# Optimization experiments

Hardware: AMD Instinct MI355X
Metric: run time of the kernel (lower is better)

Reference implementation:

```python
import jax, jax.numpy as jnp
import numpy as np

KS = 3  # kernel size (mask semantics hardcode 3x3 = 9 taps)


def _xy2d(n, x, y):
    # Hilbert curve: 2D coords -> 1D distance (exact port of HilbertTopology.xy2d)
    d = 0
    s = n // 2
    while s > 0:
        rx = 1 if (x & s) > 0 else 0
        ry = 1 if (y & s) > 0 else 0
        d += s * s * ((3 * rx) ^ ry)
        # rot(s, x, y, rx, ry)
        if ry == 0:
            if rx == 1:
                x = s - 1 - x
                y = s - 1 - y
            x, y = y, x
        s //= 2
    return d


def _build_causal_mask(height, width):
    n = 1
    while n < max(width, height):
        n *= 2
    hgrid = np.empty((height, width), dtype=np.int64)
    for y in range(height):
        for x in range(width):
            hgrid[y, x] = _xy2d(n, x, y)
    # pad with -1 so out-of-bounds neighbors never mask (mask stays 1.0, matching torch code)
    hp = np.pad(hgrid, 1, constant_values=-1)
    mask = np.ones((KS * KS, height, width), dtype=np.float32)
    k = 0
    for dy in range(KS):
        for dx in range(KS):
            nh = hp[dy:dy + height, dx:dx + width]
            mask[k] = np.where(nh > hgrid, 0.0, 1.0)
            k += 1
    return mask[None, None]  # [1, 1, 9, H, W]


def setup_inputs() -> dict:
    key = jax.random.key(0)
    k1, k2 = jax.random.split(key)
    B, C, H, W = 4, 256, 128, 128
    retina = jax.random.normal(k1, (B, C, H, W), dtype=jnp.float32)
    evolve_weight = jax.random.normal(k2, (C, C, KS, KS), dtype=jnp.float32) * 0.05
    causal_mask = jnp.asarray(_build_causal_mask(H, W))
    return {"retina": retina, "evolve_weight": evolve_weight,
            "causal_mask": causal_mask, "steps": 5}


def _spatial_causal_conv(x, evolve_weight, causal_mask):
    B, C, H, W = x.shape
    xp = jnp.pad(x, ((0, 0), (0, 0), (1, 1), (1, 1)))
    # im2col in F.unfold's (dy, dx) tap order -> [B, C, 9, H, W]
    patches = jnp.stack([xp[:, :, dy:dy + H, dx:dx + W]
                         for dy in range(KS) for dx in range(KS)], axis=2)
    masked = patches * causal_mask  # position-dependent causal mask
    w = evolve_weight.reshape(C, C * KS * KS)
    out = jnp.einsum('oj,bjhw->bohw', w, masked.reshape(B, C * KS * KS, H, W))
    return out


def reference(retina, evolve_weight, causal_mask, steps):
    x = retina
    for _ in range(steps):
        delta = _spatial_causal_conv(x, evolve_weight, causal_mask)
        x = x + delta / (1.0 + jnp.abs(delta))  # exact_activation
    return x
```

## Files before the change

### kernel.cpp

```cpp
#include <hip/hip_runtime.h>
#include <math.h>
#include <stdint.h>

#define B_ 4
#define C_ 256
#define H_ 128
#define W_ 128
#define NPIX (H_*W_)

typedef short bf16x8 __attribute__((ext_vector_type(8)));
typedef int   i32x4  __attribute__((ext_vector_type(4)));
typedef float f32x4  __attribute__((ext_vector_type(4)));
typedef float f32x16 __attribute__((ext_vector_type(16)));
typedef unsigned short u16x4 __attribute__((ext_vector_type(4)));

#define XSZ   41984
#define WOFF  (2*XSZ)
#define WSL   32768
#define SCR   (WOFF + 2*WSL)
#define LDS_TOTAL (SCR + 1024)

__device__ __forceinline__ unsigned short f2bf_rne(float v) {
    uint32_t b = __float_as_uint(v);
    return (unsigned short)((b + 0x7fff + ((b >> 16) & 1)) >> 16);
}
__device__ __forceinline__ float bf2f(unsigned short h) {
    return __uint_as_float(((uint32_t)h) << 16);
}

__global__ __launch_bounds__(256)
void prep_w(const float* __restrict__ wg, unsigned short* __restrict__ wb,
            unsigned short* __restrict__ zb) {
    if (blockIdx.x == 2304) { if (threadIdx.x < 128) zb[threadIdx.x] = 0; return; }
    int f = blockIdx.x * 256 + threadIdx.x;
    int sl = f >> 14, within = f & 16383;
    int o = within >> 6, t = within & 63;
    int up = t >> 3, e = t & 7;
    int qt = sl / 9, k = sl - qt * 9;
    int c = qt * 64 + ((up ^ (o & 7)) << 3) + e;
    wb[f] = f2bf_rne(wg[(o * C_ + c) * 9 + k]);
}

__global__ __launch_bounds__(256)
void prep_split(const float* __restrict__ retina, unsigned short* __restrict__ hi,
                unsigned short* __restrict__ lo) {
    __shared__ unsigned int t[64][65];
    int bid = blockIdx.x;
    const int wt = bid & 1;        bid >>= 1;
    const int h  = bid & 127;      bid >>= 7;
    const int ct = bid & 3;        const int b = bid >> 2;
    const int tid = threadIdx.x;
    const int ci4 = tid >> 6, wi = tid & 63;
    #pragma unroll
    for (int cc = 0; cc < 16; ++cc) {
        int c_loc = cc * 4 + ci4;
        float v = retina[((size_t)(b * C_ + ct * 64 + c_loc) * H_ + h) * W_ + wt * 64 + wi];
        unsigned short hv = f2bf_rne(v);
        unsigned short lv = f2bf_rne(v - bf2f(hv));
        t[c_loc][wi] = (unsigned)hv | ((unsigned)lv << 16);
    }
    __syncthreads();
    const int p = tid >> 2, j = tid & 3;
    size_t base = (((size_t)(b * H_ + h) * W_ + wt * 64 + p) << 8) + ct * 64 + j * 16;
    u16x4 hv4[4], lv4[4];
    #pragma unroll
    for (int e = 0; e < 16; ++e) {
        unsigned u = t[j * 16 + e][p];
        hv4[e >> 2][e & 3] = (unsigned short)(u & 0xffffu);
        lv4[e >> 2][e & 3] = (unsigned short)(u >> 16);
    }
    #pragma unroll
    for (int q2 = 0; q2 < 4; ++q2) {
        *(u16x4*)(hi + base + q2 * 4) = hv4[q2];
        *(u16x4*)(lo + base + q2 * 4) = lv4[q2];
    }
}

__device__ __forceinline__ void stage_w(const unsigned short* __restrict__ wb_all,
                                        char* smem, int woff, int sl, int wid, int l) {
    const char* src = (const char*)wb_all + ((size_t)sl << 15);
    #pragma unroll
    for (int j = 0; j < 4; ++j) {
        const int seg = ((j << 3) + wid) << 10;
        __builtin_amdgcn_global_load_lds(
            (const __attribute__((address_space(1))) uint32_t*)(src + seg + l * 16),
            (__attribute__((address_space(3))) uint32_t*)(smem + woff + seg), 16, 0, 0);
    }
    __builtin_amdgcn_sched_barrier(0);
}

__device__ __forceinline__ void stage_x(const unsigned short* __restrict__ hi_in,
                                        const unsigned short* __restrict__ zb,
                                        char* smem, int xoff, int b, int tr, int tc,
                                        int qt, int wid, int l) {
    const int slot_r = l >> 3, sub = l & 7;
    #pragma unroll
    for (int op = 0; op < 6; ++op) {
        const int sbase = (op << 6) + (wid << 3);
        const int s = sbase + slot_r;
        const int rr = (s * 3641) >> 16;
        const int hc = s - rr * 18;
        const int h = tr * 16 + rr - 1;
        const int w = tc * 16 + hc - 1;
        const unsigned short* src;
        int dst;
        if (sbase < 328) {
            dst = xoff + (sbase << 7);
            if ((unsigned)h < 128u && (unsigned)w < 128u)
                src = hi_in + ((((size_t)(b * 128 + h) << 7) + w) << 8) + (qt << 6)
                            + ((sub ^ (s & 7)) << 3);
            else
                src = zb + (sub << 3);
        } else {
            dst = SCR;
            src = zb + (sub << 3);
        }
        __builtin_amdgcn_global_load_lds(
            (const __attribute__((address_space(1))) uint32_t*)src,
            (__attribute__((address_space(3))) uint32_t*)(smem + dst), 16, 0, 0);
    }
    __builtin_amdgcn_sched_barrier(0);
}

__global__ __launch_bounds__(512, 2)
void nca_v7(const unsigned short* __restrict__ hi_in,
            const unsigned short* __restrict__ lo_in,
            const unsigned short* __restrict__ wb,
            const unsigned short* __restrict__ zb,
            const float* __restrict__ mask,
            unsigned short* __restrict__ hi_out,
            unsigned short* __restrict__ lo_out)
{
    extern __shared__ char smem[];
    const int tid = threadIdx.x;
    const int l = tid & 63, wid = tid >> 6;
    const int wave_o = wid & 1, wave_p = wid >> 1;
    const int lane31 = l & 31, khalf = l >> 5;
    const int col = l & 15, rowin = (l >> 4) & 1;

    int bid = blockIdx.x;
    const int tc = bid & 7; bid >>= 3;
    const int tr = bid & 7; const int b = bid >> 3;

    unsigned mbits = 0;
    #pragma unroll
    for (int k = 0; k < 9; ++k) {
        #pragma unroll
        for (int n = 0; n < 2; ++n) {
            const int h = tr * 16 + wave_p * 4 + n * 2 + rowin;
            const int w = tc * 16 + col;
            unsigned bit = (mask[k * NPIX + h * W_ + w] != 0.f) ? 1u : 0u;
            mbits |= bit << (k * 2 + n);
        }
    }
    __builtin_amdgcn_sched_barrier(0);

    stage_w(wb, smem, WOFF,       0, wid, l);
    stage_w(wb, smem, WOFF + WSL, 1, wid, l);
    stage_x(hi_in, zb, smem, 0,   b, tr, tc, 0, wid, l);
    stage_x(hi_in, zb, smem, XSZ, b, tr, tc, 1, wid, l);

    int sB[2];
    #pragma unroll
    for (int n = 0; n < 2; ++n) sB[n] = (wave_p * 4 + n * 2 + rowin) * 18 + col;
    int abase[4], aswz[4];
    #pragma unroll
    for (int mo = 0; mo < 4; ++mo) {
        int o_l = wave_o * 128 + mo * 32 + lane31;
        abase[mo] = o_l << 7;
        aswz[mo] = o_l & 7;
    }

    f32x16 zv;
    #pragma unroll
    for (int r = 0; r < 16; ++r) zv[r] = 0.f;
    f32x16 acc[4][2];
    #pragma unroll
    for (int mo = 0; mo < 4; ++mo)
        #pragma unroll
        for (int n = 0; n < 2; ++n) acc[mo][n] = zv;

    #pragma unroll 1
    for (int qt = 0; qt < 4; ++qt) {
        const char* xbuf = smem + ((qt & 1) ? XSZ : 0);
        #pragma unroll 1
        for (int k = 0; k < 9; ++k) {
            const int sl = qt * 9 + k;
            if (qt == 0 && k <= 1)                   asm volatile("s_waitcnt vmcnt(6)"  ::: "memory");
            else if ((qt == 1 || qt == 2) && k <= 1) asm volatile("s_waitcnt vmcnt(10)" ::: "memory");
            else if (sl == 35)                       asm volatile("s_waitcnt vmcnt(0)"  ::: "memory");
            else                                     asm volatile("s_waitcnt vmcnt(4)"  ::: "memory");
            __builtin_amdgcn_sched_barrier(0);
            __builtin_amdgcn_s_barrier();

            const int dy = (k * 11) >> 5;
            const int dx = k - dy * 3;
            const int doff = dy * 18 + dx;
            const char* wbuf = smem + WOFF + ((sl & 1) ? WSL : 0);
            const unsigned mk = mbits >> (k * 2);

            int sx[2];
            #pragma unroll
            for (int n = 0; n < 2; ++n) sx[n] = sB[n] + doff;

            __builtin_amdgcn_s_setprio(1);
            #pragma unroll
            for (int ks = 0; ks < 4; ++ks) {
                const int ua = ks * 2 + khalf;
                bf16x8 av[4];
                #pragma unroll
                for (int mo = 0; mo < 4; ++mo)
                    av[mo] = *(const bf16x8*)(wbuf + abase[mo] + ((ua ^ aswz[mo]) << 4));
                bf16x8 bv[2];
                #pragma unroll
                for (int n = 0; n < 2; ++n) {
                    i32x4 braw = *(const i32x4*)(xbuf + sx[n] * 128 + ((ua ^ (sx[n] & 7)) << 4));
                    const int mm = -(int)((mk >> n) & 1u);
                    #pragma unroll
                    for (int w4 = 0; w4 < 4; ++w4) braw[w4] &= mm;
                    bv[n] = __builtin_bit_cast(bf16x8, braw);
                }
                #pragma unroll
                for (int mo = 0; mo < 4; ++mo)
                    #pragma unroll
                    for (int n = 0; n < 2; ++n)
                        acc[mo][n] = __builtin_amdgcn_mfma_f32_32x32x16_bf16(av[mo], bv[n], acc[mo][n], 0, 0, 0);
            }
            __builtin_amdgcn_s_setprio(0);

            asm volatile("" ::: "memory");
            __builtin_amdgcn_s_barrier();
            if (sl + 2 < 36)
                stage_w(wb, smem, WOFF + ((sl & 1) ? WSL : 0), sl + 2, wid, l);
            if (k == 8 && qt < 2)
                stage_x(hi_in, zb, smem, (qt & 1) ? XSZ : 0, b, tr, tc, qt + 2, wid, l);
        }
    }

    __syncthreads();
    #pragma unroll
    for (int ph = 0; ph < 2; ++ph) {
        if ((wave_p >> 1) == ph) {
            #pragma unroll
            for (int mo = 0; mo < 4; ++mo) {
                #pragma unroll
                for (int n = 0; n < 2; ++n) {
                    const int row_local = (wave_p & 1) * 4 + n * 2 + rowin;
                    const int pl = row_local * 16 + col;
                    #pragma unroll
                    for (int rq = 0; rq < 4; ++rq) {
                        const int u = wave_o * 32 + mo * 8 + rq * 2 + khalf;
                        f32x4 v;
                        v[0] = acc[mo][n][rq * 4 + 0];
                        v[1] = acc[mo][n][rq * 4 + 1];
                        v[2] = acc[mo][n][rq * 4 + 2];
                        v[3] = acc[mo][n][rq * 4 + 3];
                        *(f32x4*)(smem + pl * 1024 + ((u ^ (pl & 7)) << 4)) = v;
                    }
                }
            }
        }
        __syncthreads();
        #pragma unroll 2
        for (int it = 0; it < 16; ++it) {
            const int pl = it * 8 + wid;
            const int h = tr * 16 + ph * 8 + (pl >> 4);
            const int w = tc * 16 + (pl & 15);
            const f32x4 d4 = *(const f32x4*)(smem + pl * 1024 + ((l ^ wid) << 4));
            const size_t base = (((size_t)((b * 128 + h) * 128 + w)) << 8) + l * 4;
            const u16x4 h4 = *(const u16x4*)(hi_in + base);
            const u16x4 l4 = *(const u16x4*)(lo_in + base);
            u16x4 ho, lo2;
            #pragma unroll
            for (int r = 0; r < 4; ++r) {
                const float xv = bf2f(h4[r]) + bf2f(l4[r]);
                const float d = d4[r];
                const float xn = xv + d / (1.f + fabsf(d));
                ho[r] = f2bf_rne(xn);
                lo2[r] = f2bf_rne(xn - bf2f(ho[r]));
            }
            *(u16x4*)(hi_out + base) = ho;
            *(u16x4*)(lo_out + base) = lo2;
        }
        if (ph == 0) __syncthreads();
    }
}

__global__ __launch_bounds__(256)
void shadows_to_f32(const unsigned short* __restrict__ hi,
                    const unsigned short* __restrict__ lo,
                    float* __restrict__ out)
{
    __shared__ float t[64][132];
    int bid = blockIdx.x;
    const int ct = bid & 3;  bid >>= 2;
    const int h  = bid & 127; const int b = bid >> 7;
    const int tid = threadIdx.x;
    #pragma unroll
    for (int pass = 0; pass < 8; ++pass) {
        const int w = pass * 16 + (tid >> 4);
        const int c0 = (tid & 15) * 4;
        const size_t base = (((size_t)((b * 128 + h) * 128 + w)) << 8) + ct * 64 + c0;
        const u16x4 hv = *(const u16x4*)(hi + base);
        const u16x4 lv = *(const u16x4*)(lo + base);
        #pragma unroll
        for (int e = 0; e < 4; ++e) t[c0 + e][w] = bf2f(hv[e]) + bf2f(lv[e]);
    }
    __syncthreads();
    #pragma unroll
    for (int pass = 0; pass < 8; ++pass) {
        const int c = pass * 8 + (tid >> 5);
        const int w = (tid & 31) * 4;
        float4 v = make_float4(t[c][w], t[c][w + 1], t[c][w + 2], t[c][w + 3]);
        *(float4*)(out + ((size_t)(b * C_ + ct * 64 + c) * H_ + h) * W_ + w) = v;
    }
}

#define OT 64
#define TR 4
#define TC 16
#define CKC 16
__global__ __launch_bounds__(256)
void nca_step_f32(const float* __restrict__ xin, const float* __restrict__ wg,
                  const float* __restrict__ mask, float* __restrict__ xout)
{
    __shared__ __align__(16) float w_s[CKC][9][OT];
    __shared__ __align__(16) float x_s[CKC][TR + 2][20];
    const int tid = threadIdx.x;
    int bt = blockIdx.x;
    const int col_tile = bt & 7;  bt >>= 3;
    const int row_tile = bt & 31; bt >>= 5;
    const int ot = bt & 3;        const int b = bt >> 2;
    const int gr0 = row_tile * TR, gc0 = col_tile * TC, o_base = ot * OT;
    const int og = tid >> 4, pg = tid & 15;
    const int prow = pg >> 2, pcol4 = (pg & 3) * 4;
    const int orow = gr0 + prow, ocol0 = gc0 + pcol4;
    float mask_r[9][4];
// ... 43 lines not shown
#pragma unroll
                    for (int j = 0; j < 4; ++j) acck[dxx][a][j] = 0.f;
#pragma unroll 4
            for (int c = 0; c < CKC; ++c) {
                const float4 xv4 = *(const float4*)&x_s[c][prow + dyy][pcol4];
                const float2 xv2 = *(const float2*)&x_s[c][prow + dyy][pcol4 + 4];
                const float xv[6] = {xv4.x, xv4.y, xv4.z, xv4.w, xv2.x, xv2.y};
#pragma unroll
                for (int dxx = 0; dxx < 3; ++dxx) {
                    const float4 wv = *(const float4*)&w_s[c][dyy * 3 + dxx][og * 4];
                    const float wa[4] = {wv.x, wv.y, wv.z, wv.w};
#pragma unroll
                    for (int a = 0; a < 4; ++a)
#pragma unroll
                        for (int j = 0; j < 4; ++j)
                            acck[dxx][a][j] = fmaf(wa[a], xv[j + dxx], acck[dxx][a][j]);
                }
            }
#pragma unroll
            for (int dxx = 0; dxx < 3; ++dxx) {
                const int k = dyy * 3 + dxx;
#pragma unroll
                for (int a = 0; a < 4; ++a)
#pragma unroll
                    for (int j = 0; j < 4; ++j)
                        acc[a][j] = fmaf(mask_r[k][j], acck[dxx][a][j], acc[a][j]);
            }
        }
        __syncthreads();
    }
#pragma unroll
    for (int a = 0; a < 4; ++a) {
        const int o = o_base + og * 4 + a;
#pragma unroll
        for (int j = 0; j < 4; ++j) {
            const int idx = ((b * C_ + o) * H_ + orow) * W_ + (ocol0 + j);
            const float d = acc[a][j];
            xout[idx] = xin[idx] + d / (1.0f + fabsf(d));
        }
    }
}

extern "C" void kernel_launch(void* const* d_in, const int* in_sizes, int n_in,
                              void* d_out, int out_size, void* d_ws, size_t ws_size,
                              hipStream_t stream) {
    const float* retina = (const float*)d_in[0];
    const float* wg     = (const float*)d_in[1];
    const float* mask   = (const float*)d_in[2];
    float* out = (float*)d_out;

    const size_t need = 0x4200000;

    if (ws_size >= need) {
        unsigned short* wb  = (unsigned short*)d_ws;
        unsigned short* zb  = (unsigned short*)((char*)d_ws + 0x120000);
        unsigned short* hiA = (unsigned short*)((char*)d_ws + 0x200000);
        unsigned short* loA = (unsigned short*)((char*)d_ws + 0x2200000);
        unsigned short* hiB = (unsigned short*)d_out;
        unsigned short* loB = hiB + (size_t)B_ * NPIX * C_;

        hipFuncSetAttribute((const void*)nca_v7,
                            hipFuncAttributeMaxDynamicSharedMemorySize, LDS_TOTAL);

        prep_w<<<2305, 256, 0, stream>>>(wg, wb, zb);
        prep_split<<<4096, 256, 0, stream>>>(retina, hiB, loB);

        nca_v7<<<256, 512, LDS_TOTAL, stream>>>(hiB, loB, wb, zb, mask, hiA, loA);
        nca_v7<<<256, 512, LDS_TOTAL, stream>>>(hiA, loA, wb, zb, mask, hiB, loB);
        nca_v7<<<256, 512, LDS_TOTAL, stream>>>(hiB, loB, wb, zb, mask, hiA, loA);
        nca_v7<<<256, 512, LDS_TOTAL, stream>>>(hiA, loA, wb, zb, mask, hiB, loB);
        nca_v7<<<256, 512, LDS_TOTAL, stream>>>(hiB, loB, wb, zb, mask, hiA, loA);
        shadows_to_f32<<<2048, 256, 0, stream>>>(hiA, loA, out);
    } else {
        float* ws = (float*)d_ws;
        const int nblocks = B_ * (C_ / OT) * (H_ / TR) * (W_ / TC);
        const float* src = retina;
        float* dsts[5] = {out, ws, out, ws, out};
        for (int s = 0; s < 5; ++s) {
            nca_step_f32<<<dim3(nblocks), dim3(256), 0, stream>>>(src, wg, mask, dsts[s]);
            src = dsts[s];
        }
    }
}
```

Measured before the change: 484.4 us.

## Load weight fragments directly into registers instead of staging through LDS

Weights are repacked into an MFMA-fragment-ready layout so each wave loads its A operands straight from global memory into registers, double-buffered two slices ahead. This removes LDS weight staging and most per-slice barriers. Waves are re-partitioned to 64 output channels by 64 pixels (2x4 MFMA tiles), and the epilogue writes in four quarter passes. The cost is higher register pressure and heavier global/L2 weight traffic per wave, plus fully unrolled code.

```diff
diff --git a/kernel.cpp b/kernel.cpp
--- a/kernel.cpp
+++ b/kernel.cpp
@@ -15,9 +15,7 @@
 typedef unsigned short u16x4 __attribute__((ext_vector_type(4)));
 
 #define XSZ   41984
-#define WOFF  (2*XSZ)
-#define WSL   32768
-#define SCR   (WOFF + 2*WSL)
+#define SCR   (2*XSZ)
 #define LDS_TOTAL (SCR + 1024)
 
 __device__ __forceinline__ unsigned short f2bf_rne(float v) {
@@ -29,16 +27,23 @@
 }
 
 __global__ __launch_bounds__(256)
-void prep_w(const float* __restrict__ wg, unsigned short* __restrict__ wb,
-            unsigned short* __restrict__ zb) {
+void prep_w2(const float* __restrict__ wg, unsigned short* __restrict__ wb2,
+             unsigned short* __restrict__ zb) {
     if (blockIdx.x == 2304) { if (threadIdx.x < 128) zb[threadIdx.x] = 0; return; }
     int f = blockIdx.x * 256 + threadIdx.x;
-    int sl = f >> 14, within = f & 16383;
-    int o = within >> 6, t = within & 63;
-    int up = t >> 3, e = t & 7;
+    int sl = f >> 14;
+    int r = f & 16383;
+    int oq = r >> 12;  r &= 4095;
+    int mo = r >> 11;  r &= 2047;
+    int ks = r >> 9;   r &= 511;
+    int kh = r >> 8;
+    int o5 = (r >> 3) & 31;
+    int e  = r & 7;
+    int o = oq * 64 + mo * 32 + o5;
+    int u = ks * 2 + kh;
     int qt = sl / 9, k = sl - qt * 9;
-    int c = qt * 64 + ((up ^ (o & 7)) << 3) + e;
-    wb[f] = f2bf_rne(wg[(o * C_ + c) * 9 + k]);
+    int c = qt * 64 + u * 8 + e;
+    wb2[f] = f2bf_rne(wg[(o * C_ + c) * 9 + k]);
 }
 
 __global__ __launch_bounds__(256)
@@ -74,19 +79,6 @@
         *(u16x4*)(hi + base + q2 * 4) = hv4[q2];
         *(u16x4*)(lo + base + q2 * 4) = lv4[q2];
     }
-}
-
-__device__ __forceinline__ void stage_w(const unsigned short* __restrict__ wb_all,
-                                        char* smem, int woff, int sl, int wid, int l) {
-    const char* src = (const char*)wb_all + ((size_t)sl << 15);
-    #pragma unroll
-    for (int j = 0; j < 4; ++j) {
-        const int seg = ((j << 3) + wid) << 10;
-        __builtin_amdgcn_global_load_lds(
-            (const __attribute__((address_space(1))) uint32_t*)(src + seg + l * 16),
-            (__attribute__((address_space(3))) uint32_t*)(smem + woff + seg), 16, 0, 0);
-    }
-    __builtin_amdgcn_sched_barrier(0);
 }
 
 __device__ __forceinline__ void stage_x(const unsigned short* __restrict__ hi_in,
@@ -122,10 +114,12 @@
     __builtin_amdgcn_sched_barrier(0);
 }
 
+struct Aset { bf16x8 f[2][4]; };
+
 __global__ __launch_bounds__(512, 2)
-void nca_v7(const unsigned short* __restrict__ hi_in,
+void nca_v8(const unsigned short* __restrict__ hi_in,
             const unsigned short* __restrict__ lo_in,
-            const unsigned short* __restrict__ wb,
+            const unsigned short* __restrict__ wb2,
             const unsigned short* __restrict__ zb,
             const float* __restrict__ mask,
             unsigned short* __restrict__ hi_out,
@@ -134,155 +128,154 @@
     extern __shared__ char smem[];
     const int tid = threadIdx.x;
     const int l = tid & 63, wid = tid >> 6;
-    const int wave_o = wid & 1, wave_p = wid >> 1;
-    const int lane31 = l & 31, khalf = l >> 5;
+    const int oq = wid & 3, ph2 = wid >> 2;
+    const int khalf = l >> 5;
     const int col = l & 15, rowin = (l >> 4) & 1;
 
     int bid = blockIdx.x;
     const int tc = bid & 7; bid >>= 3;
     const int tr = bid & 7; const int b = bid >> 3;
 
-    unsigned mbits = 0;
+    unsigned long long mbits = 0ull;
     #pragma unroll
     for (int k = 0; k < 9; ++k) {
         #pragma unroll
-        for (int n = 0; n < 2; ++n) {
-            const int h = tr * 16 + wave_p * 4 + n * 2 + rowin;
+        for (int n = 0; n < 4; ++n) {
+            const int h = tr * 16 + ph2 * 8 + n * 2 + rowin;
             const int w = tc * 16 + col;
-            unsigned bit = (mask[k * NPIX + h * W_ + w] != 0.f) ? 1u : 0u;
-            mbits |= bit << (k * 2 + n);
+            unsigned long long bit = (mask[k * NPIX + h * W_ + w] != 0.f) ? 1ull : 0ull;
+            mbits |= bit << (k * 4 + n);
         }
     }
     __builtin_amdgcn_sched_barrier(0);
 
-    stage_w(wb, smem, WOFF,       0, wid, l);
-    stage_w(wb, smem, WOFF + WSL, 1, wid, l);
     stage_x(hi_in, zb, smem, 0,   b, tr, tc, 0, wid, l);
     stage_x(hi_in, zb, smem, XSZ, b, tr, tc, 1, wid, l);
 
-    int sB[2];
-    #pragma unroll
-    for (int n = 0; n < 2; ++n) sB[n] = (wave_p * 4 + n * 2 + rowin) * 18 + col;
-    int abase[4], aswz[4];
-    #pragma unroll
-    for (int mo = 0; mo < 4; ++mo) {
-        int o_l = wave_o * 128 + mo * 32 + lane31;
-        abase[mo] = o_l << 7;
-        aswz[mo] = o_l & 7;
-    }
+    const char* abase = (const char*)wb2 + (oq << 13) + (l << 4);
+    Aset a0, a1;
+    #pragma unroll
+    for (int mo = 0; mo < 2; ++mo)
+        #pragma unroll
+        for (int ks = 0; ks < 4; ++ks) {
+            a0.f[mo][ks] = *(const bf16x8*)(abase +     0 + mo * 4096 + ks * 1024);
+            a1.f[mo][ks] = *(const bf16x8*)(abase + 32768 + mo * 4096 + ks * 1024);
+        }
+    asm volatile("s_waitcnt vmcnt(16)" ::: "memory");
+    __builtin_amdgcn_sched_barrier(0);
+    __builtin_amdgcn_s_barrier();
+
+    int sB[4];
+    #pragma unroll
+    for (int n = 0; n < 4; ++n) sB[n] = (ph2 * 8 + n * 2 + rowin) * 18 + col;
 
     f32x16 zv;
     #pragma unroll
     for (int r = 0; r < 16; ++r) zv[r] = 0.f;
-    f32x16 acc[4][2];
-    #pragma unroll
-    for (int mo = 0; mo < 4; ++mo)
+    f32x16 acc[2][4];
+    #pragma unroll
+    for (int mo = 0; mo < 2; ++mo)
         #pragma unroll
-        for (int n = 0; n < 2; ++n) acc[mo][n] = zv;
-
-    #pragma unroll 1
-    for (int qt = 0; qt < 4; ++qt) {
+        for (int n = 0; n < 4; ++n) acc[mo][n] = zv;
+
+    #pragma unroll
+    for (int sl = 0; sl < 36; ++sl) {
+        const int qt = sl / 9, k = sl - qt * 9;
+        const int dy = k / 3, dx = k - dy * 3;
+        const int doff = dy * 18 + dx;
         const char* xbuf = smem + ((qt & 1) ? XSZ : 0);
-        #pragma unroll 1
-        for (int k = 0; k < 9; ++k) {
-            const int sl = qt * 9 + k;
-            if (qt == 0 && k <= 1)                   asm volatile("s_waitcnt vmcnt(6)"  ::: "memory");
-            else if ((qt == 1 || qt == 2) && k <= 1) asm volatile("s_waitcnt vmcnt(10)" ::: "memory");
-            else if (sl == 35)                       asm volatile("s_waitcnt vmcnt(0)"  ::: "memory");
-            else                                     asm volatile("s_waitcnt vmcnt(4)"  ::: "memory");
+        const unsigned mk = (unsigned)(mbits >> (k * 4));
+        Aset& cur = (sl & 1) ? a1 : a0;
+
+        __builtin_amdgcn_s_setprio(1);
+        #pragma unroll
+        for (int ks = 0; ks < 4; ++ks) {
+            const int u = ks * 2 + khalf;
+            bf16x8 bv[4];
+            #pragma unroll
+            for (int n = 0; n < 4; ++n) {
+                const int spx = sB[n] + doff;
+                i32x4 braw = *(const i32x4*)(xbuf + spx * 128 + ((u ^ (spx & 7)) << 4));
+                const int mm = -(int)((mk >> n) & 1u);
+                #pragma unroll
+                for (int w4 = 0; w4 < 4; ++w4) braw[w4] &= mm;
+                bv[n] = __builtin_bit_cast(bf16x8, braw);
+            }
+            #pragma unroll
+            for (int mo = 0; mo < 2; ++mo)
+                #pragma unroll
+                for (int n = 0; n < 4; ++n)
+                    acc[mo][n] = __builtin_amdgcn_mfma_f32_32x32x16_bf16(cur.f[mo][ks], bv[n], acc[mo][n], 0, 0, 0);
+        }
+        __builtin_amdgcn_s_setprio(0);
+
+        if (sl + 2 < 36) {
+            const char* base2 = abase + (size_t)(sl + 2) * 32768;
+            #pragma unroll
+            for (int mo = 0; mo < 2; ++mo)
+                #pragma unroll
+                for (int ks = 0; ks < 4; ++ks)
+                    cur.f[mo][ks] = *(const bf16x8*)(base2 + mo * 4096 + ks * 1024);
+        }
+        if (k == 4 && (qt == 1 || qt == 2))
+            stage_x(hi_in, zb, smem, ((qt + 1) & 1) ? XSZ : 0, b, tr, tc, qt + 1, wid, l);
+        if (k == 8 && qt < 3) {
+            __builtin_amdgcn_sched_barrier(0);
+            if (qt >= 1) { asm volatile("s_waitcnt vmcnt(24)" ::: "memory"); }
             __builtin_amdgcn_sched_barrier(0);
             __builtin_amdgcn_s_barrier();
-
-            const int dy = (k * 11) >> 5;
-            const int dx = k - dy * 3;
-            const int doff = dy * 18 + dx;
-            const char* wbuf = smem + WOFF + ((sl & 1) ? WSL : 0);
-            const unsigned mk = mbits >> (k * 2);
-
-            int sx[2];
+        }
+    }
+
+    __syncthreads();
+    #pragma unroll 1
+    for (int f = 0; f < 4; ++f) {
+        if (ph2 == (f >> 1)) {
             #pragma unroll
-            for (int n = 0; n < 2; ++n) sx[n] = sB[n] + doff;
-
-            __builtin_amdgcn_s_setprio(1);
-            #pragma unroll
-            for (int ks = 0; ks < 4; ++ks) {
-                const int ua = ks * 2 + khalf;
-                bf16x8 av[4];
+            for (int nn = 0; nn < 2; ++nn) {
+                const int n = (f & 1) * 2 + nn;
+                const int px = (nn * 2 + rowin) * 16 + col;
                 #pragma unroll
-                for (int mo = 0; mo < 4; ++mo)
-                    av[mo] = *(const bf16x8*)(wbuf + abase[mo] + ((ua ^ aswz[mo]) << 4));
-                bf16x8 bv[2];
-                #pragma unroll
-                for (int n = 0; n < 2; ++n) {
-                    i32x4 braw = *(const i32x4*)(xbuf + sx[n] * 128 + ((ua ^ (sx[n] & 7)) << 4));
-                    const int mm = -(int)((mk >> n) & 1u);
-                    #pragma unroll
-                    for (int w4 = 0; w4 < 4; ++w4) braw[w4] &= mm;
-                    bv[n] = __builtin_bit_cast(bf16x8, braw);
-                }
-                #pragma unroll
-                for (int mo = 0; mo < 4; ++mo)
-                    #pragma unroll
-                    for (int n = 0; n < 2; ++n)
-                        acc[mo][n] = __builtin_amdgcn_mfma_f32_32x32x16_bf16(av[mo], bv[n], acc[mo][n], 0, 0, 0);
-            }
-            __builtin_amdgcn_s_setprio(0);
-
-            asm volatile("" ::: "memory");
-            __builtin_amdgcn_s_barrier();
-            if (sl + 2 < 36)
-                stage_w(wb, smem, WOFF + ((sl & 1) ? WSL : 0), sl + 2, wid, l);
-            if (k == 8 && qt < 2)
-                stage_x(hi_in, zb, smem, (qt & 1) ? XSZ : 0, b, tr, tc, qt + 2, wid, l);
-        }
-    }
-
-    __syncthreads();
-    #pragma unroll
-    for (int ph = 0; ph < 2; ++ph) {
-        if ((wave_p >> 1) == ph) {
-            #pragma unroll
-            for (int mo = 0; mo < 4; ++mo) {
-                #pragma unroll
-                for (int n = 0; n < 2; ++n) {
-                    const int row_local = (wave_p & 1) * 4 + n * 2 + rowin;
-                    const int pl = row_local * 16 + col;
+                for (int mo = 0; mo < 2; ++mo)
                     #pragma unroll
                     for (int rq = 0; rq < 4; ++rq) {
-                        const int u = wave_o * 32 + mo * 8 + rq * 2 + khalf;
+                        const int u = oq * 16 + mo * 8 + rq * 2 + khalf;
                         f32x4 v;
                         v[0] = acc[mo][n][rq * 4 + 0];
                         v[1] = acc[mo][n][rq * 4 + 1];
                         v[2] = acc[mo][n][rq * 4 + 2];
                         v[3] = acc[mo][n][rq * 4 + 3];
-                        *(f32x4*)(smem + pl * 1024 + ((u ^ (pl & 7)) << 4)) = v;
+                        *(f32x4*)(smem + px * 1024 + ((u ^ (px & 7)) << 4)) = v;
                     }
+            }
+        }
+        __syncthreads();
+        {
+            const int px = tid >> 3, q = tid & 7;
+            const int h = tr * 16 + f * 4 + (px >> 4);
+            const int w = tc * 16 + (px & 15);
+            const size_t pixbase = ((size_t)((b * 128 + h) * 128 + w)) << 8;
+            #pragma unroll
+            for (int j = 0; j < 8; ++j) {
+                const int u = q + 8 * j;
+                const f32x4 d4 = *(const f32x4*)(smem + px * 1024 + ((u ^ (px & 7)) << 4));
+                const size_t a2 = pixbase + 4 * (size_t)u;
+                const u16x4 h4 = *(const u16x4*)(hi_in + a2);
+                const u16x4 l4 = *(const u16x4*)(lo_in + a2);
+                u16x4 ho, lo2;
+                #pragma unroll
+                for (int r = 0; r < 4; ++r) {
+                    const float xv = bf2f(h4[r]) + bf2f(l4[r]);
+                    const float d = d4[r];
+                    const float xn = xv + d / (1.f + fabsf(d));
+                    ho[r] = f2bf_rne(xn);
+                    lo2[r] = f2bf_rne(xn - bf2f(ho[r]));
                 }
-            }
-        }
-        __syncthreads();
-        #pragma unroll 2
-        for (int it = 0; it < 16; ++it) {
-            const int pl = it * 8 + wid;
-            const int h = tr * 16 + ph * 8 + (pl >> 4);
-            const int w = tc * 16 + (pl & 15);
-            const f32x4 d4 = *(const f32x4*)(smem + pl * 1024 + ((l ^ wid) << 4));
-            const size_t base = (((size_t)((b * 128 + h) * 128 + w)) << 8) + l * 4;
-            const u16x4 h4 = *(const u16x4*)(hi_in + base);
-            const u16x4 l4 = *(const u16x4*)(lo_in + base);
-            u16x4 ho, lo2;
-            #pragma unroll
-            for (int r = 0; r < 4; ++r) {
-                const float xv = bf2f(h4[r]) + bf2f(l4[r]);
-                const float d = d4[r];
-                const float xn = xv + d / (1.f + fabsf(d));
-                ho[r] = f2bf_rne(xn);
-                lo2[r] = f2bf_rne(xn - bf2f(ho[r]));
-            }
-            *(u16x4*)(hi_out + base) = ho;
-            *(u16x4*)(lo_out + base) = lo2;
-        }
-        if (ph == 0) __syncthreads();
+                *(u16x4*)(hi_out + a2) = ho;
+                *(u16x4*)(lo_out + a2) = lo2;
+            }
+        }
+        if (f < 3) __syncthreads();
     }
 }
 
@@ -432,24 +425,24 @@
     const size_t need = 0x4200000;
 
     if (ws_size >= need) {
-        unsigned short* wb  = (unsigned short*)d_ws;
+        unsigned short* wb2 = (unsigned short*)d_ws;
         unsigned short* zb  = (unsigned short*)((char*)d_ws + 0x120000);
         unsigned short* hiA = (unsigned short*)((char*)d_ws + 0x200000);
         unsigned short* loA = (unsigned short*)((char*)d_ws + 0x2200000);
         unsigned short* hiB = (unsigned short*)d_out;
         unsigned short* loB = hiB + (size_t)B_ * NPIX * C_;
 
-        hipFuncSetAttribute((const void*)nca_v7,
+        hipFuncSetAttribute((const void*)nca_v8,
                             hipFuncAttributeMaxDynamicSharedMemorySize, LDS_TOTAL);
 
-        prep_w<<<2305, 256, 0, stream>>>(wg, wb, zb);
+        prep_w2<<<2305, 256, 0, stream>>>(wg, wb2, zb);
         prep_split<<<4096, 256, 0, stream>>>(retina, hiB, loB);
 
-        nca_v7<<<256, 512, LDS_TOTAL, stream>>>(hiB, loB, wb, zb, mask, hiA, loA);
-        nca_v7<<<256, 512, LDS_TOTAL, stream>>>(hiA, loA, wb, zb, mask, hiB, loB);
-        nca_v7<<<256, 512, LDS_TOTAL, stream>>>(hiB, loB, wb, zb, mask, hiA, loA);
-        nca_v7<<<256, 512, LDS_TOTAL, stream>>>(hiA, loA, wb, zb, mask, hiB, loB);
-        nca_v7<<<256, 512, LDS_TOTAL, stream>>>(hiB, loB, wb, zb, mask, hiA, loA);
+        nca_v8<<<256, 512, LDS_TOTAL, stream>>>(hiB, loB, wb2, zb, mask, hiA, loA);
+        nca_v8<<<256, 512, LDS_TOTAL, stream>>>(hiA, loA, wb2, zb, mask, hiB, loB);
+        nca_v8<<<256, 512, LDS_TOTAL, stream>>>(hiB, loB, wb2, zb, mask, hiA, loA);
+        nca_v8<<<256, 512, LDS_TOTAL, stream>>>(hiA, loA, wb2, zb, mask, hiB, loB);
+        nca_v8<<<256, 512, LDS_TOTAL, stream>>>(hiB, loB, wb2, zb, mask, hiA, loA);
         shadows_to_f32<<<2048, 256, 0, stream>>>(hiA, loA, out);
     } else {
         float* ws = (float*)d_ws;
```

Result: slower. 947.3 us (+95.5%).

## Halve spatial tile and channel slice to shrink LDS and double blocks

Applied to the files above, without the earlier changes.

The conv kernel now uses a 16x8 pixel tile with 256 threads instead of 16x16 with 512. Channels are staged in 32-channel slices over 8 passes instead of 64-channel slices over 4, with the weight pre-swizzle, LDS layout and wait counts reworked to match. This cuts LDS per block to about 65KB and launches 512 blocks, aiming for more resident blocks per CU and better load balance across the 256 CUs. In exchange there are more barriers and pipeline stages per channel, and the halo overhead per output pixel is higher; the epilogue is also rewritten to use 8-wide vector stores.

```diff
diff --git a/kernel.cpp b/kernel.cpp
--- a/kernel.cpp
+++ b/kernel.cpp
@@ -13,12 +13,13 @@
 typedef float f32x4  __attribute__((ext_vector_type(4)));
 typedef float f32x16 __attribute__((ext_vector_type(16)));
 typedef unsigned short u16x4 __attribute__((ext_vector_type(4)));
-
-#define XSZ   41984
-#define WOFF  (2*XSZ)
-#define WSL   32768
-#define SCR   (WOFF + 2*WSL)
-#define LDS_TOTAL (SCR + 1024)
+typedef unsigned short u16x8 __attribute__((ext_vector_type(8)));
+
+#define XSL  192
+#define XSZ2 (XSL*64)
+#define WOFF (2*XSZ2)
+#define WSL2 16384
+#define LDS_TOTAL 66560
 
 __device__ __forceinline__ unsigned short f2bf_rne(float v) {
     uint32_t b = __float_as_uint(v);
@@ -29,16 +30,19 @@
 }
 
 __global__ __launch_bounds__(256)
-void prep_w(const float* __restrict__ wg, unsigned short* __restrict__ wb,
-            unsigned short* __restrict__ zb) {
+void prep_w3(const float* __restrict__ wg, unsigned short* __restrict__ wb3,
+             unsigned short* __restrict__ zb) {
     if (blockIdx.x == 2304) { if (threadIdx.x < 128) zb[threadIdx.x] = 0; return; }
     int f = blockIdx.x * 256 + threadIdx.x;
-    int sl = f >> 14, within = f & 16383;
-    int o = within >> 6, t = within & 63;
+    int sl = f >> 13;
+    int r = f & 8191;
+    int o = r >> 5;
+    int t = r & 31;
     int up = t >> 3, e = t & 7;
-    int qt = sl / 9, k = sl - qt * 9;
-    int c = qt * 64 + ((up ^ (o & 7)) << 3) + e;
-    wb[f] = f2bf_rne(wg[(o * C_ + c) * 9 + k]);
+    int cq = sl / 9, k = sl - cq * 9;
+    int u = up ^ (o & 3);
+    int c = cq * 32 + u * 8 + e;
+    wb3[f] = f2bf_rne(wg[(o * C_ + c) * 9 + k]);
 }
 
 __global__ __launch_bounds__(256)
@@ -76,12 +80,12 @@
     }
 }
 
-__device__ __forceinline__ void stage_w(const unsigned short* __restrict__ wb_all,
-                                        char* smem, int woff, int sl, int wid, int l) {
-    const char* src = (const char*)wb_all + ((size_t)sl << 15);
+__device__ __forceinline__ void stage_w2(const unsigned short* __restrict__ wb3,
+                                         char* smem, int woff, int sl, int wid, int l) {
+    const char* src = (const char*)wb3 + ((size_t)sl << 14);
     #pragma unroll
     for (int j = 0; j < 4; ++j) {
-        const int seg = ((j << 3) + wid) << 10;
+        const int seg = ((j << 2) + wid) << 10;
         __builtin_amdgcn_global_load_lds(
             (const __attribute__((address_space(1))) uint32_t*)(src + seg + l * 16),
             (__attribute__((address_space(3))) uint32_t*)(smem + woff + seg), 16, 0, 0);
@@ -89,43 +93,37 @@
     __builtin_amdgcn_sched_barrier(0);
 }
 
-__device__ __forceinline__ void stage_x(const unsigned short* __restrict__ hi_in,
-                                        const unsigned short* __restrict__ zb,
-                                        char* smem, int xoff, int b, int tr, int tc,
-                                        int qt, int wid, int l) {
-    const int slot_r = l >> 3, sub = l & 7;
-    #pragma unroll
-    for (int op = 0; op < 6; ++op) {
-        const int sbase = (op << 6) + (wid << 3);
+__device__ __forceinline__ void stage_x2(const unsigned short* __restrict__ hi_in,
+                                         const unsigned short* __restrict__ zb,
+                                         char* smem, int xoff, int b, int tr, int tc,
+                                         int cq, int wid, int l) {
+    const int slot_r = l >> 2, sub = l & 3;
+    #pragma unroll
+    for (int op = 0; op < 3; ++op) {
+        const int sbase = ((op << 2) + wid) << 4;
         const int s = sbase + slot_r;
         const int rr = (s * 3641) >> 16;
         const int hc = s - rr * 18;
-        const int h = tr * 16 + rr - 1;
+        const int h = tr * 8 + rr - 1;
         const int w = tc * 16 + hc - 1;
         const unsigned short* src;
-        int dst;
-        if (sbase < 328) {
-            dst = xoff + (sbase << 7);
-            if ((unsigned)h < 128u && (unsigned)w < 128u)
-                src = hi_in + ((((size_t)(b * 128 + h) << 7) + w) << 8) + (qt << 6)
-                            + ((sub ^ (s & 7)) << 3);
-            else
-                src = zb + (sub << 3);
-        } else {
-            dst = SCR;
+        if (s < 180 && (unsigned)h < 128u && (unsigned)w < 128u)
+            src = hi_in + (((size_t)((b * 128 + h) * 128 + w)) << 8) + (cq << 5)
+                        + ((sub ^ (s & 3)) << 3);
+        else
             src = zb + (sub << 3);
-        }
         __builtin_amdgcn_global_load_lds(
             (const __attribute__((address_space(1))) uint32_t*)src,
-            (__attribute__((address_space(3))) uint32_t*)(smem + dst), 16, 0, 0);
+            (__attribute__((address_space(3))) uint32_t*)(smem + xoff + (sbase << 6)),
+            16, 0, 0);
     }
     __builtin_amdgcn_sched_barrier(0);
 }
 
-__global__ __launch_bounds__(512, 2)
-void nca_v7(const unsigned short* __restrict__ hi_in,
+__global__ __launch_bounds__(256, 2)
+void nca_v9(const unsigned short* __restrict__ hi_in,
             const unsigned short* __restrict__ lo_in,
-            const unsigned short* __restrict__ wb,
+            const unsigned short* __restrict__ wb3,
             const unsigned short* __restrict__ zb,
             const float* __restrict__ mask,
             unsigned short* __restrict__ hi_out,
@@ -140,14 +138,14 @@
 
     int bid = blockIdx.x;
     const int tc = bid & 7; bid >>= 3;
-    const int tr = bid & 7; const int b = bid >> 3;
+    const int tr = bid & 15; const int b = bid >> 4;
 
     unsigned mbits = 0;
     #pragma unroll
     for (int k = 0; k < 9; ++k) {
         #pragma unroll
         for (int n = 0; n < 2; ++n) {
-            const int h = tr * 16 + wave_p * 4 + n * 2 + rowin;
+            const int h = tr * 8 + wave_p * 4 + n * 2 + rowin;
             const int w = tc * 16 + col;
             unsigned bit = (mask[k * NPIX + h * W_ + w] != 0.f) ? 1u : 0u;
             mbits |= bit << (k * 2 + n);
@@ -155,10 +153,10 @@
     }
     __builtin_amdgcn_sched_barrier(0);
 
-    stage_w(wb, smem, WOFF,       0, wid, l);
-    stage_w(wb, smem, WOFF + WSL, 1, wid, l);
-    stage_x(hi_in, zb, smem, 0,   b, tr, tc, 0, wid, l);
-    stage_x(hi_in, zb, smem, XSZ, b, tr, tc, 1, wid, l);
+    stage_w2(wb3, smem, WOFF,        0, wid, l);
+    stage_w2(wb3, smem, WOFF + WSL2, 1, wid, l);
+    stage_x2(hi_in, zb, smem, 0,     b, tr, tc, 0, wid, l);
+    stage_x2(hi_in, zb, smem, XSZ2,  b, tr, tc, 1, wid, l);
 
     int sB[2];
     #pragma unroll
@@ -167,8 +165,8 @@
     #pragma unroll
     for (int mo = 0; mo < 4; ++mo) {
         int o_l = wave_o * 128 + mo * 32 + lane31;
-        abase[mo] = o_l << 7;
-        aswz[mo] = o_l & 7;
+        abase[mo] = o_l << 6;
+        aswz[mo] = o_l & 3;
     }
 
     f32x16 zv;
@@ -181,22 +179,22 @@
         for (int n = 0; n < 2; ++n) acc[mo][n] = zv;
 
     #pragma unroll 1
-    for (int qt = 0; qt < 4; ++qt) {
-        const char* xbuf = smem + ((qt & 1) ? XSZ : 0);
+    for (int cq = 0; cq < 8; ++cq) {
+        const char* xbuf = smem + ((cq & 1) ? XSZ2 : 0);
         #pragma unroll 1
         for (int k = 0; k < 9; ++k) {
-            const int sl = qt * 9 + k;
-            if (qt == 0 && k <= 1)                   asm volatile("s_waitcnt vmcnt(6)"  ::: "memory");
-            else if ((qt == 1 || qt == 2) && k <= 1) asm volatile("s_waitcnt vmcnt(10)" ::: "memory");
-            else if (sl == 35)                       asm volatile("s_waitcnt vmcnt(0)"  ::: "memory");
-            else                                     asm volatile("s_waitcnt vmcnt(4)"  ::: "memory");
+            const int sl = cq * 9 + k;
+            if (sl == 0)       asm volatile("s_waitcnt vmcnt(3)" ::: "memory");
+            else if (sl == 71) asm volatile("s_waitcnt vmcnt(0)" ::: "memory");
+            else if (k <= 1)   asm volatile("s_waitcnt vmcnt(7)" ::: "memory");
+            else               asm volatile("s_waitcnt vmcnt(4)" ::: "memory");
             __builtin_amdgcn_sched_barrier(0);
             __builtin_amdgcn_s_barrier();
 
             const int dy = (k * 11) >> 5;
             const int dx = k - dy * 3;
             const int doff = dy * 18 + dx;
-            const char* wbuf = smem + WOFF + ((sl & 1) ? WSL : 0);
+            const char* wbuf = smem + WOFF + ((sl & 1) ? WSL2 : 0);
             const unsigned mk = mbits >> (k * 2);
 
             int sx[2];
@@ -205,16 +203,16 @@
 
             __builtin_amdgcn_s_setprio(1);
             #pragma unroll
-            for (int ks = 0; ks < 4; ++ks) {
-                const int ua = ks * 2 + khalf;
+            for (int ks = 0; ks < 2; ++ks) {
+                const int u = ks * 2 + khalf;
                 bf16x8 av[4];
                 #pragma unroll
                 for (int mo = 0; mo < 4; ++mo)
-                    av[mo] = *(const bf16x8*)(wbuf + abase[mo] + ((ua ^ aswz[mo]) << 4));
+                    av[mo] = *(const bf16x8*)(wbuf + abase[mo] + ((u ^ aswz[mo]) << 4));
                 bf16x8 bv[2];
                 #pragma unroll
                 for (int n = 0; n < 2; ++n) {
-                    i32x4 braw = *(const i32x4*)(xbuf + sx[n] * 128 + ((ua ^ (sx[n] & 7)) << 4));
+                    i32x4 braw = *(const i32x4*)(xbuf + (sx[n] << 6) + ((u ^ (sx[n] & 3)) << 4));
                     const int mm = -(int)((mk >> n) & 1u);
                     #pragma unroll
                     for (int w4 = 0; w4 < 4; ++w4) braw[w4] &= mm;
@@ -230,59 +228,58 @@
 
             asm volatile("" ::: "memory");
             __builtin_amdgcn_s_barrier();
-            if (sl + 2 < 36)
-                stage_w(wb, smem, WOFF + ((sl & 1) ? WSL : 0), sl + 2, wid, l);
-            if (k == 8 && qt < 2)
-                stage_x(hi_in, zb, smem, (qt & 1) ? XSZ : 0, b, tr, tc, qt + 2, wid, l);
+            if (sl + 2 < 72)
+                stage_w2(wb3, smem, WOFF + ((sl & 1) ? WSL2 : 0), sl + 2, wid, l);
+            if (k == 8 && cq < 6)
+                stage_x2(hi_in, zb, smem, (cq & 1) ? XSZ2 : 0, b, tr, tc, cq + 2, wid, l);
         }
     }
 
     __syncthreads();
-    #pragma unroll
-    for (int ph = 0; ph < 2; ++ph) {
-        if ((wave_p >> 1) == ph) {
+    #pragma unroll 1
+    for (int n = 0; n < 2; ++n) {
+        const int pl = (wave_p * 2 + rowin) * 16 + col;
+        #pragma unroll
+        for (int mo = 0; mo < 4; ++mo)
             #pragma unroll
-            for (int mo = 0; mo < 4; ++mo) {
+            for (int rq = 0; rq < 4; ++rq) {
+                const int u = wave_o * 32 + mo * 8 + rq * 2 + khalf;
+                f32x4 v;
+                v[0] = acc[mo][n][rq * 4 + 0];
+                v[1] = acc[mo][n][rq * 4 + 1];
+                v[2] = acc[mo][n][rq * 4 + 2];
+                v[3] = acc[mo][n][rq * 4 + 3];
+                *(f32x4*)(smem + pl * 1024 + ((u ^ (pl & 7)) << 4)) = v;
+            }
+        __syncthreads();
+        {
+            const int pl2 = tid >> 2, q = tid & 3;
+            const int pr = pl2 >> 4;
+            const int h = tr * 8 + (pr >> 1) * 4 + n * 2 + (pr & 1);
+            const int w = tc * 16 + (pl2 & 15);
+            const size_t pixbase = ((size_t)((b * 128 + h) * 128 + w)) << 8;
+            #pragma unroll
+            for (int j = 0; j < 8; ++j) {
+                const int u0 = q * 2 + j * 8;
+                const f32x4 d0 = *(const f32x4*)(smem + pl2 * 1024 + ((u0 ^ (pl2 & 7)) << 4));
+                const f32x4 d1 = *(const f32x4*)(smem + pl2 * 1024 + (((u0 + 1) ^ (pl2 & 7)) << 4));
+                const size_t a2 = pixbase + (size_t)u0 * 4;
+                const u16x8 h8 = *(const u16x8*)(hi_in + a2);
+                const u16x8 l8 = *(const u16x8*)(lo_in + a2);
+                u16x8 ho, lo2;
                 #pragma unroll
-                for (int n = 0; n < 2; ++n) {
-                    const int row_local = (wave_p & 1) * 4 + n * 2 + rowin;
-                    const int pl = row_local * 16 + col;
-                    #pragma unroll
-                    for (int rq = 0; rq < 4; ++rq) {
-                        const int u = wave_o * 32 + mo * 8 + rq * 2 + khalf;
-                        f32x4 v;
-                        v[0] = acc[mo][n][rq * 4 + 0];
-                        v[1] = acc[mo][n][rq * 4 + 1];
-                        v[2] = acc[mo][n][rq * 4 + 2];
-                        v[3] = acc[mo][n][rq * 4 + 3];
-                        *(f32x4*)(smem + pl * 1024 + ((u ^ (pl & 7)) << 4)) = v;
-                    }
+                for (int r = 0; r < 8; ++r) {
+                    const float dd = (r < 4) ? d0[r] : d1[r - 4];
+                    const float xv = bf2f(h8[r]) + bf2f(l8[r]);
+                    const float xn = xv + dd / (1.f + fabsf(dd));
+                    ho[r] = f2bf_rne(xn);
+                    lo2[r] = f2bf_rne(xn - bf2f(ho[r]));
                 }
+                *(u16x8*)(hi_out + a2) = ho;
+                *(u16x8*)(lo_out + a2) = lo2;
             }
         }
         __syncthreads();
-        #pragma unroll 2
-        for (int it = 0; it < 16; ++it) {
-            const int pl = it * 8 + wid;
-            const int h = tr * 16 + ph * 8 + (pl >> 4);
-            const int w = tc * 16 + (pl & 15);
-            const f32x4 d4 = *(const f32x4*)(smem + pl * 1024 + ((l ^ wid) << 4));
-            const size_t base = (((size_t)((b * 128 + h) * 128 + w)) << 8) + l * 4;
-            const u16x4 h4 = *(const u16x4*)(hi_in + base);
-            const u16x4 l4 = *(const u16x4*)(lo_in + base);
-            u16x4 ho, lo2;
-            #pragma unroll
-            for (int r = 0; r < 4; ++r) {
-                const float xv = bf2f(h4[r]) + bf2f(l4[r]);
-                const float d = d4[r];
-                const float xn = xv + d / (1.f + fabsf(d));
-                ho[r] = f2bf_rne(xn);
-                lo2[r] = f2bf_rne(xn - bf2f(ho[r]));
-            }
-            *(u16x4*)(hi_out + base) = ho;
-            *(u16x4*)(lo_out + base) = lo2;
-        }
-        if (ph == 0) __syncthreads();
     }
 }
 
@@ -432,24 +429,24 @@
     const size_t need = 0x4200000;
 
     if (ws_size >= need) {
-        unsigned short* wb  = (unsigned short*)d_ws;
+        unsigned short* wb3 = (unsigned short*)d_ws;
         unsigned short* zb  = (unsigned short*)((char*)d_ws + 0x120000);
         unsigned short* hiA = (unsigned short*)((char*)d_ws + 0x200000);
         unsigned short* loA = (unsigned short*)((char*)d_ws + 0x2200000);
         unsigned short* hiB = (unsigned short*)d_out;
         unsigned short* loB = hiB + (size_t)B_ * NPIX * C_;
 
-        hipFuncSetAttribute((const void*)nca_v7,
+        hipFuncSetAttribute((const void*)nca_v9,
                             hipFuncAttributeMaxDynamicSharedMemorySize, LDS_TOTAL);
 
-        prep_w<<<2305, 256, 0, stream>>>(wg, wb, zb);
+        prep_w3<<<2305, 256, 0, stream>>>(wg, wb3, zb);
         prep_split<<<4096, 256, 0, stream>>>(retina, hiB, loB);
 
-        nca_v7<<<256, 512, LDS_TOTAL, stream>>>(hiB, loB, wb, zb, mask, hiA, loA);
-        nca_v7<<<256, 512, LDS_TOTAL, stream>>>(hiA, loA, wb, zb, mask, hiB, loB);
-        nca_v7<<<256, 512, LDS_TOTAL, stream>>>(hiB, loB, wb, zb, mask, hiA, loA);
-        nca_v7<<<256, 512, LDS_TOTAL, stream>>>(hiA, loA, wb, zb, mask, hiB, loB);
-        nca_v7<<<256, 512, LDS_TOTAL, stream>>>(hiB, loB, wb, zb, mask, hiA, loA);
+        nca_v9<<<512, 256, LDS_TOTAL, stream>>>(hiB, loB, wb3, zb, mask, hiA, loA);
+        nca_v9<<<512, 256, LDS_TOTAL, stream>>>(hiA, loA, wb3, zb, mask, hiB, loB);
+        nca_v9<<<512, 256, LDS_TOTAL, stream>>>(hiB, loB, wb3, zb, mask, hiA, loA);
+        nca_v9<<<512, 256, LDS_TOTAL, stream>>>(hiA, loA, wb3, zb, mask, hiB, loB);
+        nca_v9<<<512, 256, LDS_TOTAL, stream>>>(hiB, loB, wb3, zb, mask, hiA, loA);
         shadows_to_f32<<<2048, 256, 0, stream>>>(hiA, loA, out);
     } else {
         float* ws = (float*)d_ws;
```

After: 645.9 us. +33.3%, slower.

## Double block to 16 waves, halving per-wave output-channel tiles

Applied to the files above, without the earlier changes.

The conv kernel now launches 1024 threads per block instead of 512. Each wave owns 64 output channels (2 MFMA row tiles) rather than 128, and staging loops, waitcnt thresholds and epilogue indexing are rescaled to the new wave count. The aim is more resident waves per CU to hide LDS and global latency, at the cost of less A/B fragment reuse per wave and more barrier participants. Register pressure drops from the smaller accumulator set, but the launch-bound occupancy hint may not be reachable given LDS usage per block.

```diff
diff --git a/kernel.cpp b/kernel.cpp
--- a/kernel.cpp
+++ b/kernel.cpp
@@ -76,12 +76,12 @@
     }
 }
 
-__device__ __forceinline__ void stage_w(const unsigned short* __restrict__ wb_all,
+__device__ __forceinline__ void stage_w(const unsigned short* __restrict__ wb,
                                         char* smem, int woff, int sl, int wid, int l) {
-    const char* src = (const char*)wb_all + ((size_t)sl << 15);
-    #pragma unroll
-    for (int j = 0; j < 4; ++j) {
-        const int seg = ((j << 3) + wid) << 10;
+    const char* src = (const char*)wb + ((size_t)sl << 15);
+    #pragma unroll
+    for (int op = 0; op < 2; ++op) {
+        const int seg = ((op << 4) + wid) << 10;
         __builtin_amdgcn_global_load_lds(
             (const __attribute__((address_space(1))) uint32_t*)(src + seg + l * 16),
             (__attribute__((address_space(3))) uint32_t*)(smem + woff + seg), 16, 0, 0);
@@ -91,12 +91,13 @@
 
 __device__ __forceinline__ void stage_x(const unsigned short* __restrict__ hi_in,
                                         const unsigned short* __restrict__ zb,
-                                        char* smem, int xoff, int b, int tr, int tc,
+                                        char* smem, int b, int tr, int tc,
                                         int qt, int wid, int l) {
     const int slot_r = l >> 3, sub = l & 7;
-    #pragma unroll
-    for (int op = 0; op < 6; ++op) {
-        const int sbase = (op << 6) + (wid << 3);
+    const int xoff = (qt & 1) ? XSZ : 0;
+    #pragma unroll
+    for (int op = 0; op < 3; ++op) {
+        const int sbase = ((op << 4) + wid) << 3;
         const int s = sbase + slot_r;
         const int rr = (s * 3641) >> 16;
         const int hc = s - rr * 18;
@@ -106,8 +107,8 @@
         int dst;
         if (sbase < 328) {
             dst = xoff + (sbase << 7);
-            if ((unsigned)h < 128u && (unsigned)w < 128u)
-                src = hi_in + ((((size_t)(b * 128 + h) << 7) + w) << 8) + (qt << 6)
+            if (s < 324 && (unsigned)h < 128u && (unsigned)w < 128u)
+                src = hi_in + (((size_t)((b * 128 + h) * 128 + w)) << 8) + (qt << 6)
                             + ((sub ^ (s & 7)) << 3);
             else
                 src = zb + (sub << 3);
@@ -122,19 +123,19 @@
     __builtin_amdgcn_sched_barrier(0);
 }
 
-__global__ __launch_bounds__(512, 2)
-void nca_v7(const unsigned short* __restrict__ hi_in,
-            const unsigned short* __restrict__ lo_in,
-            const unsigned short* __restrict__ wb,
-            const unsigned short* __restrict__ zb,
-            const float* __restrict__ mask,
-            unsigned short* __restrict__ hi_out,
-            unsigned short* __restrict__ lo_out)
+__global__ __launch_bounds__(1024, 4)
+void nca_v12(const unsigned short* __restrict__ hi_in,
+             const unsigned short* __restrict__ lo_in,
+             const unsigned short* __restrict__ wb,
+             const unsigned short* __restrict__ zb,
+             const float* __restrict__ mask,
+             unsigned short* __restrict__ hi_out,
+             unsigned short* __restrict__ lo_out)
 {
     extern __shared__ char smem[];
     const int tid = threadIdx.x;
     const int l = tid & 63, wid = tid >> 6;
-    const int wave_o = wid & 1, wave_p = wid >> 1;
+    const int og = wid & 3, ph = wid >> 2;
     const int lane31 = l & 31, khalf = l >> 5;
     const int col = l & 15, rowin = (l >> 4) & 1;
 
@@ -147,7 +148,7 @@
     for (int k = 0; k < 9; ++k) {
         #pragma unroll
         for (int n = 0; n < 2; ++n) {
-            const int h = tr * 16 + wave_p * 4 + n * 2 + rowin;
+            const int h = tr * 16 + ph * 4 + n * 2 + rowin;
             const int w = tc * 16 + col;
             unsigned bit = (mask[k * NPIX + h * W_ + w] != 0.f) ? 1u : 0u;
             mbits |= bit << (k * 2 + n);
@@ -157,16 +158,16 @@
 
     stage_w(wb, smem, WOFF,       0, wid, l);
     stage_w(wb, smem, WOFF + WSL, 1, wid, l);
-    stage_x(hi_in, zb, smem, 0,   b, tr, tc, 0, wid, l);
-    stage_x(hi_in, zb, smem, XSZ, b, tr, tc, 1, wid, l);
+    stage_x(hi_in, zb, smem, b, tr, tc, 0, wid, l);
+    stage_x(hi_in, zb, smem, b, tr, tc, 1, wid, l);
 
     int sB[2];
     #pragma unroll
-    for (int n = 0; n < 2; ++n) sB[n] = (wave_p * 4 + n * 2 + rowin) * 18 + col;
-    int abase[4], aswz[4];
-    #pragma unroll
-    for (int mo = 0; mo < 4; ++mo) {
-        int o_l = wave_o * 128 + mo * 32 + lane31;
+    for (int n = 0; n < 2; ++n) sB[n] = (ph * 4 + n * 2 + rowin) * 18 + col;
+    int abase[2], aswz[2];
+    #pragma unroll
+    for (int mo = 0; mo < 2; ++mo) {
+        int o_l = og * 64 + mo * 32 + lane31;
         abase[mo] = o_l << 7;
         aswz[mo] = o_l & 7;
     }
@@ -174,9 +175,9 @@
     f32x16 zv;
     #pragma unroll
     for (int r = 0; r < 16; ++r) zv[r] = 0.f;
-    f32x16 acc[4][2];
-    #pragma unroll
-    for (int mo = 0; mo < 4; ++mo)
+    f32x16 acc[2][2];
+    #pragma unroll
+    for (int mo = 0; mo < 2; ++mo)
         #pragma unroll
         for (int n = 0; n < 2; ++n) acc[mo][n] = zv;
 
@@ -186,10 +187,11 @@
         #pragma unroll 1
         for (int k = 0; k < 9; ++k) {
             const int sl = qt * 9 + k;
-            if (qt == 0 && k <= 1)                   asm volatile("s_waitcnt vmcnt(6)"  ::: "memory");
-            else if ((qt == 1 || qt == 2) && k <= 1) asm volatile("s_waitcnt vmcnt(10)" ::: "memory");
-            else if (sl == 35)                       asm volatile("s_waitcnt vmcnt(0)"  ::: "memory");
-            else                                     asm volatile("s_waitcnt vmcnt(4)"  ::: "memory");
+            if (sl == 0)                          asm volatile("s_waitcnt vmcnt(3)" ::: "memory");
+            else if (sl == 1)                     asm volatile("s_waitcnt vmcnt(5)" ::: "memory");
+            else if (k <= 1 && qt >= 1 && qt <= 2) asm volatile("s_waitcnt vmcnt(5)" ::: "memory");
+            else if (sl == 35)                    asm volatile("s_waitcnt vmcnt(0)" ::: "memory");
+            else                                  asm volatile("s_waitcnt vmcnt(2)" ::: "memory");
             __builtin_amdgcn_sched_barrier(0);
             __builtin_amdgcn_s_barrier();
 
@@ -207,21 +209,21 @@
             #pragma unroll
             for (int ks = 0; ks < 4; ++ks) {
                 const int ua = ks * 2 + khalf;
-                bf16x8 av[4];
+                bf16x8 av[2];
                 #pragma unroll
-                for (int mo = 0; mo < 4; ++mo)
+                for (int mo = 0; mo < 2; ++mo)
                     av[mo] = *(const bf16x8*)(wbuf + abase[mo] + ((ua ^ aswz[mo]) << 4));
                 bf16x8 bv[2];
                 #pragma unroll
                 for (int n = 0; n < 2; ++n) {
-                    i32x4 braw = *(const i32x4*)(xbuf + sx[n] * 128 + ((ua ^ (sx[n] & 7)) << 4));
+                    i32x4 braw = *(const i32x4*)(xbuf + (sx[n] << 7) + ((ua ^ (sx[n] & 7)) << 4));
                     const int mm = -(int)((mk >> n) & 1u);
                     #pragma unroll
                     for (int w4 = 0; w4 < 4; ++w4) braw[w4] &= mm;
                     bv[n] = __builtin_bit_cast(bf16x8, braw);
                 }
                 #pragma unroll
-                for (int mo = 0; mo < 4; ++mo)
+                for (int mo = 0; mo < 2; ++mo)
                     #pragma unroll
                     for (int n = 0; n < 2; ++n)
                         acc[mo][n] = __builtin_amdgcn_mfma_f32_32x32x16_bf16(av[mo], bv[n], acc[mo][n], 0, 0, 0);
@@ -233,23 +235,23 @@
             if (sl + 2 < 36)
                 stage_w(wb, smem, WOFF + ((sl & 1) ? WSL : 0), sl + 2, wid, l);
             if (k == 8 && qt < 2)
-                stage_x(hi_in, zb, smem, (qt & 1) ? XSZ : 0, b, tr, tc, qt + 2, wid, l);
+                stage_x(hi_in, zb, smem, b, tr, tc, qt + 2, wid, l);
         }
     }
 
     __syncthreads();
-    #pragma unroll
-    for (int ph = 0; ph < 2; ++ph) {
-        if ((wave_p >> 1) == ph) {
+    #pragma unroll 1
+    for (int f = 0; f < 2; ++f) {
+        if ((ph >> 1) == f) {
             #pragma unroll
-            for (int mo = 0; mo < 4; ++mo) {
+            for (int n = 0; n < 2; ++n) {
+                const int lrow = (ph & 1) * 4 + n * 2 + rowin;
+                const int pl = lrow * 16 + col;
                 #pragma unroll
-                for (int n = 0; n < 2; ++n) {
-                    const int row_local = (wave_p & 1) * 4 + n * 2 + rowin;
-                    const int pl = row_local * 16 + col;
+                for (int mo = 0; mo < 2; ++mo)
                     #pragma unroll
                     for (int rq = 0; rq < 4; ++rq) {
-                        const int u = wave_o * 32 + mo * 8 + rq * 2 + khalf;
+                        const int u = og * 16 + mo * 8 + rq * 2 + khalf;
                         f32x4 v;
                         v[0] = acc[mo][n][rq * 4 + 0];
                         v[1] = acc[mo][n][rq * 4 + 1];
@@ -257,16 +259,15 @@
                         v[3] = acc[mo][n][rq * 4 + 3];
                         *(f32x4*)(smem + pl * 1024 + ((u ^ (pl & 7)) << 4)) = v;
                     }
-                }
             }
         }
         __syncthreads();
-        #pragma unroll 2
-        for (int it = 0; it < 16; ++it) {
-            const int pl = it * 8 + wid;
-            const int h = tr * 16 + ph * 8 + (pl >> 4);
+        #pragma unroll
+        for (int it = 0; it < 8; ++it) {
+            const int pl = it * 16 + wid;
+            const int h = tr * 16 + f * 8 + (pl >> 4);
             const int w = tc * 16 + (pl & 15);
-            const f32x4 d4 = *(const f32x4*)(smem + pl * 1024 + ((l ^ wid) << 4));
+            const f32x4 d4 = *(const f32x4*)(smem + pl * 1024 + ((l ^ (pl & 7)) << 4));
             const size_t base = (((size_t)((b * 128 + h) * 128 + w)) << 8) + l * 4;
             const u16x4 h4 = *(const u16x4*)(hi_in + base);
             const u16x4 l4 = *(const u16x4*)(lo_in + base);
@@ -282,7 +283,7 @@
             *(u16x4*)(hi_out + base) = ho;
             *(u16x4*)(lo_out + base) = lo2;
         }
-        if (ph == 0) __syncthreads();
+        if (f == 0) __syncthreads();
     }
 }
 
@@ -439,17 +440,17 @@
         unsigned short* hiB = (unsigned short*)d_out;
         unsigned short* loB = hiB + (size_t)B_ * NPIX * C_;
 
-        hipFuncSetAttribute((const void*)nca_v7,
+        hipFuncSetAttribute((const void*)nca_v12,
                             hipFuncAttributeMaxDynamicSharedMemorySize, LDS_TOTAL);
 
         prep_w<<<2305, 256, 0, stream>>>(wg, wb, zb);
         prep_split<<<4096, 256, 0, stream>>>(retina, hiB, loB);
 
-        nca_v7<<<256, 512, LDS_TOTAL, stream>>>(hiB, loB, wb, zb, mask, hiA, loA);
-        nca_v7<<<256, 512, LDS_TOTAL, stream>>>(hiA, loA, wb, zb, mask, hiB, loB);
-        nca_v7<<<256, 512, LDS_TOTAL, stream>>>(hiB, loB, wb, zb, mask, hiA, loA);
-        nca_v7<<<256, 512, LDS_TOTAL, stream>>>(hiA, loA, wb, zb, mask, hiB, loB);
-        nca_v7<<<256, 512, LDS_TOTAL, stream>>>(hiB, loB, wb, zb, mask, hiA, loA);
+        nca_v12<<<256, 1024, LDS_TOTAL, stream>>>(hiB, loB, wb, zb, mask, hiA, loA);
+        nca_v12<<<256, 1024, LDS_TOTAL, stream>>>(hiA, loA, wb, zb, mask, hiB, loB);
+        nca_v12<<<256, 1024, LDS_TOTAL, stream>>>(hiB, loB, wb, zb, mask, hiA, loA);
+        nca_v12<<<256, 1024, LDS_TOTAL, stream>>>(hiA, loA, wb, zb, mask, hiB, loB);
+        nca_v12<<<256, 1024, LDS_TOTAL, stream>>>(hiB, loB, wb, zb, mask, hiA, loA);
         shadows_to_f32<<<2048, 256, 0, stream>>>(hiA, loA, out);
     } else {
         float* ws = (float*)d_ws;
```

After: 500.6 us. 3.3% more time.
